# Kernel optimization log

Measured on AMD Instinct MI355X. Metric: run time of the kernel, lower is better.

The kernel has to match this reference:

```python
import jax, jax.numpy as jnp
import numpy as np

EPS = 1e-7

def _attend(x):
    # x: [nc, w, h]; faithful to SelfAttention_1 with patch_size=3 (1x1 kernels, padding=1)
    nc, w, h = x.shape
    L = w * h
    # per-location 1x1 kernels, L2-normalized (kernels are [L, nc, 1, 1] in torch)
    k = x.reshape(nc, L).T + EPS                      # [L, nc]
    k = k / jnp.sqrt(jnp.sum(k * k, axis=1, keepdims=True))
    # conv2d with 1x1 kernels and padding=1 -> scores on padded grid [L, w+2, h+2]
    xp = jnp.pad(x, ((0, 0), (1, 1), (1, 1)))
    s = jnp.einsum('lc,cuv->luv', k, xp)              # [L, w+2, h+2]
    # avg_pool2d(3,1,pad=1) * 9 == 3x3 sum pooling with zero padding
    s = jax.lax.reduce_window(s, 0.0, jax.lax.add, (1, 3, 3), (1, 1, 1),
                              ((0, 0), (1, 1), (1, 1)))
    a = jax.nn.softmax(s, axis=0)                     # softmax over L (channel) axis
    # conv_transpose2d with 1x1 kernels, padding=1 == crop border then K^T @ A
    out = jnp.einsum('lc,luv->cuv', k, a[:, 1:-1, 1:-1])  # [nc, w, h]
    # torch: attention_scores.permute(0,2,3,1).view(w*h, -1) (raw reshape)
    att = jnp.transpose(a, (1, 2, 0)).reshape(L, -1)  # [L, (w+2)*(h+2)]
    return out, att


def setup_inputs() -> dict:
    key = jax.random.key(0)
    foreground = jax.random.normal(key, (4, 256, 64, 64), dtype=jnp.float32)
    return {"foreground": foreground}


def reference(foreground):
    out, att = jax.vmap(_attend)(foreground)          # out: [bz,nc,w,h], att: [bz,L,(w+2)*(h+2)]
    bz, L, M = att.shape
    return out, att.reshape(bz * L, M)
```

## Files before the change

### kernel.cpp

```cpp
#include <hip/hip_runtime.h>
#include <math.h>
#include <stdint.h>

#define LDIM 4096
#define NC   256
#define W66  66
#define P66  4356
#define BZ   4
#define EPSK 1e-7f

typedef _Float16 v8h __attribute__((ext_vector_type(8)));
typedef float v4f __attribute__((ext_vector_type(4)));

__device__ __forceinline__ void cp16(const void* g, void* l) {
    __builtin_amdgcn_global_load_lds(
        (const __attribute__((address_space(1))) void*)g,
        (__attribute__((address_space(3))) void*)l, 16, 0, 0);
}

__global__ __launch_bounds__(256) void rnorm_kernel(const float* __restrict__ x,
                                                    float* __restrict__ rnorm) {
    int idx = blockIdx.x * 256 + threadIdx.x;
    int b = idx >> 12;
    int l = idx & (LDIM - 1);
    const float* xb = x + (size_t)b * NC * LDIM + l;
    float s = 0.f;
#pragma unroll 8
    for (int c = 0; c < NC; ++c) {
        float v = xb[(size_t)c * LDIM] + EPSK;
        s += v * v;
    }
    rnorm[idx] = 1.0f / sqrtf(s);
}

__global__ __launch_bounds__(256) void kconv_kernel(const float* __restrict__ x,
                                                    const float* __restrict__ rn,
                                                    _Float16* __restrict__ Kcl,
                                                    _Float16* __restrict__ Klc) {
    __shared__ _Float16 t[64][72];
    int b = blockIdx.z, c0 = blockIdx.y * 64, l0 = blockIdx.x * 64;
    int tid = threadIdx.x;
    int r = tid >> 2, q = (tid & 3) * 16;
    const float* xr = x + ((size_t)(b * NC + c0 + r)) * LDIM + l0 + q;
    const float* rr = rn + b * LDIM + l0 + q;
    _Float16 h[16];
#pragma unroll
    for (int j = 0; j < 16; ++j)
        h[j] = (_Float16)((xr[j] + EPSK) * rr[j]);
    _Float16* kc = Kcl + ((size_t)(b * NC + c0 + r)) * LDIM + l0 + q;
    *(v8h*)kc = *(v8h*)h;
    *(v8h*)(kc + 8) = *(v8h*)(h + 8);
#pragma unroll
    for (int j = 0; j < 16; ++j) t[r][q + j] = h[j];
    __syncthreads();
    _Float16 g[16];
#pragma unroll
    for (int j = 0; j < 16; ++j) g[j] = t[q + j][r];
    _Float16* kl = Klc + ((size_t)(b * LDIM + l0 + r)) * NC + c0 + q;
    *(v8h*)kl = *(v8h*)g;
    *(v8h*)(kl + 8) = *(v8h*)(g + 8);
}

__global__ __launch_bounds__(256) void pool_kernel(const float* __restrict__ x,
                                                   float* __restrict__ Pm) {
    size_t idx = (size_t)blockIdx.x * 256 + threadIdx.x;
    int p = (int)(idx % P66);
    size_t bc = idx / P66;
    int u = p / W66, v = p % W66;
    const float* xbc = x + bc * (size_t)LDIM;
    int i0 = max(u - 2, 0), i1 = min(u, 63);
    int j0 = max(v - 2, 0), j1 = min(v, 63);
    float s = 0.f;
    for (int i = i0; i <= i1; ++i)
        for (int j = j0; j <= j1; ++j)
            s += xbc[i * 64 + j];
    Pm[idx] = s;
}

__global__ __launch_bounds__(256) void ptrans_kernel(const float* __restrict__ PoolF,
                                                     _Float16* __restrict__ Pm16) {
    __shared__ float t[64][65];
    int b = blockIdx.z, c0 = blockIdx.y * 64, p0 = blockIdx.x * 64;
    int tid = threadIdx.x;
    int r = tid >> 2, q = (tid & 3) * 16;
    const float* src = PoolF + ((size_t)(b * NC + c0 + r)) * P66 + p0 + q;
#pragma unroll
    for (int j = 0; j < 16; ++j) t[r][q + j] = src[j];
    __syncthreads();
    if (p0 + r < P66) {
        _Float16 g[16];
#pragma unroll
        for (int j = 0; j < 16; ++j) g[j] = (_Float16)t[q + j][r];
        _Float16* dst = Pm16 + ((size_t)(b * P66 + p0 + r)) * NC + c0 + q;
        *(v8h*)dst = *(v8h*)g;
        *(v8h*)(dst + 8) = *(v8h*)(g + 8);
    }
}

__global__ __launch_bounds__(256) void gemm1_mfma(const _Float16* __restrict__ Pm16,
                                                  const _Float16* __restrict__ Klc,
                                                  float* __restrict__ S) {
    __shared__ _Float16 As[128 * 32];
    __shared__ _Float16 Bs[128 * 32];
    int b = blockIdx.z;
    int p0 = blockIdx.y * 128;
    int l0 = blockIdx.x * 128;
    const _Float16* A = Pm16 + (size_t)b * P66 * NC;
    const _Float16* B = Klc + (size_t)b * LDIM * NC;
    float* C = S + (size_t)b * P66 * LDIM;
    int tid = threadIdx.x;
    int lane = tid & 63, wave = tid >> 6;
    int wm = (wave >> 1) * 64, wn = (wave & 1) * 64;
    int quad = lane >> 4, hn = lane & 15;
    int sr = tid >> 2, sk = (tid & 3) * 8;
    int pa0 = p0 + sr;      if (pa0 > P66 - 1) pa0 = P66 - 1;
    int pa1 = p0 + sr + 64; if (pa1 > P66 - 1) pa1 = P66 - 1;
    const _Float16* Ag0 = A + (size_t)pa0 * NC + sk;
    const _Float16* Ag1 = A + (size_t)pa1 * NC + sk;
    const _Float16* Bg0 = B + (size_t)(l0 + sr) * NC + sk;
    const _Float16* Bg1 = B + (size_t)(l0 + sr + 64) * NC + sk;
    char* lA = (char*)As + tid * 16;
    char* lB = (char*)Bs + tid * 16;
    v4f acc[4][4];
    v4f vz = {0.f, 0.f, 0.f, 0.f};
#pragma unroll
    for (int i = 0; i < 4; ++i)
#pragma unroll
        for (int j = 0; j < 4; ++j) acc[i][j] = vz;

    for (int k0 = 0; k0 < NC; k0 += 32) {
        __syncthreads();
        cp16(Ag0 + k0, lA);
        cp16(Ag1 + k0, lA + 4096);
        cp16(Bg0 + k0, lB);
        cp16(Bg1 + k0, lB + 4096);
        __syncthreads();
        v8h af[4], bfr[4];
#pragma unroll
        for (int t = 0; t < 4; ++t)
            af[t] = *(const v8h*)(As + (wm + t * 16 + hn) * 32 + quad * 8);
#pragma unroll
        for (int t = 0; t < 4; ++t)
            bfr[t] = *(const v8h*)(Bs + (wn + t * 16 + hn) * 32 + quad * 8);
#pragma unroll
        for (int i = 0; i < 4; ++i)
#pragma unroll
            for (int j = 0; j < 4; ++j)
                acc[i][j] = __builtin_amdgcn_mfma_f32_16x16x32_f16(af[i], bfr[j], acc[i][j], 0, 0, 0);
    }
#pragma unroll
    for (int i = 0; i < 4; ++i) {
        int pr = p0 + wm + i * 16 + quad * 4;
#pragma unroll
        for (int j = 0; j < 4; ++j) {
            int lc = l0 + wn + j * 16 + hn;
            float* Cp = C + (size_t)pr * LDIM + lc;
#pragma unroll
            for (int r = 0; r < 4; ++r)
                if (pr + r < P66) Cp[(size_t)r * LDIM] = acc[i][j][r];
        }
    }
}

__global__ __launch_bounds__(256) void softmax_kernel(float* __restrict__ att) {
    float* row = att + (size_t)blockIdx.x * LDIM;
    int tid = threadIdx.x;
    float4 v[4];
    float mx = -1e30f;
#pragma unroll
    for (int i = 0; i < 4; ++i) {
        v[i] = ((float4*)row)[tid + i * 256];
        mx = fmaxf(mx, fmaxf(fmaxf(v[i].x, v[i].y), fmaxf(v[i].z, v[i].w)));
    }
    __shared__ float sred[4];
    __shared__ float ssum[4];
#pragma unroll
    for (int off = 32; off > 0; off >>= 1) mx = fmaxf(mx, __shfl_xor(mx, off));
    if ((tid & 63) == 0) sred[tid >> 6] = mx;
    __syncthreads();
    float m4 = fmaxf(fmaxf(sred[0], sred[1]), fmaxf(sred[2], sred[3]));
    float sum = 0.f;
#pragma unroll
    for (int i = 0; i < 4; ++i) {
        v[i].x = __expf(v[i].x - m4);
        v[i].y = __expf(v[i].y - m4);
        v[i].z = __expf(v[i].z - m4);
        v[i].w = __expf(v[i].w - m4);
        sum += (v[i].x + v[i].y) + (v[i].z + v[i].w);
    }
#pragma unroll
    for (int off = 32; off > 0; off >>= 1) sum += __shfl_xor(sum, off);
    if ((tid & 63) == 0) ssum[tid >> 6] = sum;
    __syncthreads();
    float r = 1.0f / (ssum[0] + ssum[1] + ssum[2] + ssum[3]);
#pragma unroll
    for (int i = 0; i < 4; ++i) {
        v[i].x *= r; v[i].y *= r; v[i].z *= r; v[i].w *= r;
        ((float4*)row)[tid + i * 256] = v[i];
    }
}

__global__ __launch_bounds__(256) void gemm2_mfma(const _Float16* __restrict__ Kcl,
                                                  const float* __restrict__ attF,
                                                  float* __restrict__ outp) {
    __shared__ _Float16 As[128 * 32];
    __shared__ float BsF[128 * 32];
    int b = blockIdx.z;
    int c0 = blockIdx.y * 128;
    int i0 = blockIdx.x * 128;
    const _Float16* A = Kcl + (size_t)b * NC * LDIM;
    const float* Batt = attF + (size_t)b * P66 * LDIM;
    float* C = outp + (size_t)b * NC * LDIM;
    int tid = threadIdx.x;
    int lane = tid & 63, wave = tid >> 6;
    int wm = (wave >> 1) * 64, wn = (wave & 1) * 64;
    int quad = lane >> 4, hn = lane & 15;
    int sr = tid >> 2, sk = (tid & 3) * 8;
    const _Float16* Ag0 = A + (size_t)(c0 + sr) * LDIM + sk;
    const _Float16* Ag1 = A + (size_t)(c0 + sr + 64) * LDIM + sk;
    int br = tid >> 3, bo = (tid & 7) * 4;
    const float* Bg[4];
#pragma unroll
    for (int ch = 0; ch < 4; ++ch) {
        int ii = i0 + ch * 32 + br;
        int p = ((ii >> 6) + 1) * W66 + (ii & 63) + 1;
        Bg[ch] = Batt + (size_t)p * LDIM + bo;
    }
    char* lA = (char*)As + tid * 16;
    char* lB = (char*)BsF + tid * 16;
    v4f acc[4][4];
    v4f vz = {0.f, 0.f, 0.f, 0.f};
#pragma unroll
    for (int i = 0; i < 4; ++i)
#pragma unroll
        for (int j = 0; j < 4; ++j) acc[i][j] = vz;

    for (int k0 = 0; k0 < LDIM; k0 += 32) {
        __syncthreads();
        cp16(Ag0 + k0, lA);
        cp16(Ag1 + k0, lA + 4096);
#pragma unroll
        for (int ch = 0; ch < 4; ++ch)
            cp16(Bg[ch] + k0, lB + ch * 4096);
        __syncthreads();
        v8h af[4], bfr[4];
#pragma unroll
        for (int t = 0; t < 4; ++t)
            af[t] = *(const v8h*)(As + (wm + t * 16 + hn) * 32 + quad * 8);
#pragma unroll
        for (int t = 0; t < 4; ++t) {
            const float* bp = BsF + (wn + t * 16 + hn) * 32 + quad * 8;
            v4f x0 = *(const v4f*)bp;
            v4f x1 = *(const v4f*)(bp + 4);
            v8h h;
#pragma unroll
            for (int j = 0; j < 4; ++j) { h[j] = (_Float16)x0[j]; h[j + 4] = (_Float16)x1[j]; }
            bfr[t] = h;
        }
#pragma unroll
        for (int i = 0; i < 4; ++i)
#pragma unroll
            for (int j = 0; j < 4; ++j)
                acc[i][j] = __builtin_amdgcn_mfma_f32_16x16x32_f16(af[i], bfr[j], acc[i][j], 0, 0, 0);
    }
#pragma unroll
    for (int i = 0; i < 4; ++i) {
        int cr = c0 + wm + i * 16 + quad * 4;
#pragma unroll
        for (int j = 0; j < 4; ++j) {
            int ic = i0 + wn + j * 16 + hn;
            float* Cp = C + (size_t)cr * LDIM + ic;
#pragma unroll
            for (int r = 0; r < 4; ++r)
                Cp[(size_t)r * LDIM] = acc[i][j][r];
        }
    }
}

extern "C" void kernel_launch(void* const* d_in, const int* in_sizes, int n_in,
                              void* d_out, int out_size, void* d_ws, size_t ws_size,
                              hipStream_t stream) {
    const float* x = (const float*)d_in[0];
    float* out = (float*)d_out;
    float* att = (float*)d_out + 4194304;
    float* rn = (float*)d_ws;
    _Float16* Kcl = (_Float16*)(rn + 16384);
    _Float16* Klc = Kcl + (size_t)BZ * NC * LDIM;
    float* PoolF = (float*)(Klc + (size_t)BZ * NC * LDIM);
    _Float16* Pm16 = (_Float16*)(PoolF + (size_t)BZ * NC * P66);

    rnorm_kernel<<<64, 256, 0, stream>>>(x, rn);
    kconv_kernel<<<dim3(64, 4, BZ), 256, 0, stream>>>(x, rn, Kcl, Klc);
    pool_kernel<<<17424, 256, 0, stream>>>(x, PoolF);
    ptrans_kernel<<<dim3(69, 4, BZ), 256, 0, stream>>>(PoolF, Pm16);
    gemm1_mfma<<<dim3(32, 35, BZ), 256, 0, stream>>>(Pm16, Klc, att);
    softmax_kernel<<<17424, 256, 0, stream>>>(att);
    gemm2_mfma<<<dim3(32, 2, BZ), 256, 0, stream>>>(Kcl, att, out);
}
```

Before: 672.9 us.

## Shrink gemm2 N-tile to 32 with swizzled LDS for more blocks

The second GEMM now uses 128x32 output tiles instead of 128x128, so its grid grows from 256 to 1024 blocks. The grid is reordered so the two channel tiles sharing an attention slice run next to each other. The fp32 B tile in LDS gets an XOR swizzle to cut bank conflicts, and each wave now holds only four accumulators, which lowers register pressure. The cost is less data reuse: each attention element is loaded twice and the fp16 K matrix is reloaded by four times as many blocks, so global traffic and issue overhead per MFMA rise.

```diff
diff --git a/kernel.cpp b/kernel.cpp
--- a/kernel.cpp
+++ b/kernel.cpp
@@ -204,76 +204,62 @@
                                                   const float* __restrict__ attF,
                                                   float* __restrict__ outp) {
     __shared__ _Float16 As[128 * 32];
-    __shared__ float BsF[128 * 32];
+    __shared__ float BsF[32 * 32];
     int b = blockIdx.z;
-    int c0 = blockIdx.y * 128;
-    int i0 = blockIdx.x * 128;
+    int c0 = blockIdx.x * 128;
+    int i0 = blockIdx.y * 32;
     const _Float16* A = Kcl + (size_t)b * NC * LDIM;
     const float* Batt = attF + (size_t)b * P66 * LDIM;
     float* C = outp + (size_t)b * NC * LDIM;
     int tid = threadIdx.x;
     int lane = tid & 63, wave = tid >> 6;
-    int wm = (wave >> 1) * 64, wn = (wave & 1) * 64;
+    int wm = (wave >> 1) * 64, wn = (wave & 1) * 16;
     int quad = lane >> 4, hn = lane & 15;
     int sr = tid >> 2, sk = (tid & 3) * 8;
     const _Float16* Ag0 = A + (size_t)(c0 + sr) * LDIM + sk;
     const _Float16* Ag1 = A + (size_t)(c0 + sr + 64) * LDIM + sk;
-    int br = tid >> 3, bo = (tid & 7) * 4;
-    const float* Bg[4];
-#pragma unroll
-    for (int ch = 0; ch < 4; ++ch) {
-        int ii = i0 + ch * 32 + br;
-        int p = ((ii >> 6) + 1) * W66 + (ii & 63) + 1;
-        Bg[ch] = Batt + (size_t)p * LDIM + bo;
-    }
+    int br = tid >> 3;
+    int bo = (((tid & 7) ^ (br & 7)) << 2);
+    int ii = i0 + br;
+    int p = ((ii >> 6) + 1) * W66 + (ii & 63) + 1;
+    const float* Bg = Batt + (size_t)p * LDIM + bo;
     char* lA = (char*)As + tid * 16;
     char* lB = (char*)BsF + tid * 16;
-    v4f acc[4][4];
+    v4f acc[4];
     v4f vz = {0.f, 0.f, 0.f, 0.f};
 #pragma unroll
-    for (int i = 0; i < 4; ++i)
-#pragma unroll
-        for (int j = 0; j < 4; ++j) acc[i][j] = vz;
+    for (int i = 0; i < 4; ++i) acc[i] = vz;
 
     for (int k0 = 0; k0 < LDIM; k0 += 32) {
         __syncthreads();
         cp16(Ag0 + k0, lA);
         cp16(Ag1 + k0, lA + 4096);
-#pragma unroll
-        for (int ch = 0; ch < 4; ++ch)
-            cp16(Bg[ch] + k0, lB + ch * 4096);
-        __syncthreads();
-        v8h af[4], bfr[4];
+        cp16(Bg + k0, lB);
+        __syncthreads();
+        v8h af[4];
 #pragma unroll
         for (int t = 0; t < 4; ++t)
             af[t] = *(const v8h*)(As + (wm + t * 16 + hn) * 32 + quad * 8);
-#pragma unroll
-        for (int t = 0; t < 4; ++t) {
-            const float* bp = BsF + (wn + t * 16 + hn) * 32 + quad * 8;
-            v4f x0 = *(const v4f*)bp;
-            v4f x1 = *(const v4f*)(bp + 4);
-            v8h h;
-#pragma unroll
-            for (int j = 0; j < 4; ++j) { h[j] = (_Float16)x0[j]; h[j + 4] = (_Float16)x1[j]; }
-            bfr[t] = h;
-        }
+        int brow = wn + hn;
+        int s0 = ((quad * 2 + 0) ^ (brow & 7)) << 2;
+        int s1 = ((quad * 2 + 1) ^ (brow & 7)) << 2;
+        v4f x0 = *(const v4f*)(BsF + brow * 32 + s0);
+        v4f x1 = *(const v4f*)(BsF + brow * 32 + s1);
+        v8h bfr;
+#pragma unroll
+        for (int j = 0; j < 4; ++j) { bfr[j] = (_Float16)x0[j]; bfr[j + 4] = (_Float16)x1[j]; }
 #pragma unroll
         for (int i = 0; i < 4; ++i)
-#pragma unroll
-            for (int j = 0; j < 4; ++j)
-                acc[i][j] = __builtin_amdgcn_mfma_f32_16x16x32_f16(af[i], bfr[j], acc[i][j], 0, 0, 0);
+            acc[i] = __builtin_amdgcn_mfma_f32_16x16x32_f16(af[i], bfr, acc[i], 0, 0, 0);
     }
 #pragma unroll
     for (int i = 0; i < 4; ++i) {
         int cr = c0 + wm + i * 16 + quad * 4;
-#pragma unroll
-        for (int j = 0; j < 4; ++j) {
-            int ic = i0 + wn + j * 16 + hn;
-            float* Cp = C + (size_t)cr * LDIM + ic;
-#pragma unroll
-            for (int r = 0; r < 4; ++r)
-                Cp[(size_t)r * LDIM] = acc[i][j][r];
-        }
+        int ic = i0 + wn + hn;
+        float* Cp = C + (size_t)cr * LDIM + ic;
+#pragma unroll
+        for (int r = 0; r < 4; ++r)
+            Cp[(size_t)r * LDIM] = acc[i][r];
     }
 }
 
@@ -295,5 +281,5 @@
     ptrans_kernel<<<dim3(69, 4, BZ), 256, 0, stream>>>(PoolF, Pm16);
     gemm1_mfma<<<dim3(32, 35, BZ), 256, 0, stream>>>(Pm16, Klc, att);
     softmax_kernel<<<17424, 256, 0, stream>>>(att);
-    gemm2_mfma<<<dim3(32, 2, BZ), 256, 0, stream>>>(Kcl, att, out);
-}
+    gemm2_mfma<<<dim3(2, 128, BZ), 256, 0, stream>>>(Kcl, att, out);
+}
```

Result: faster. 658.0 us (-2.2%).
